# Optimization experiments

Measured on AMD Instinct MI355X. Metric: run time of the kernel, lower is better.

Reference implementation:

```python
import jax, jax.numpy as jnp
import numpy as np

N_HEAD = 12
N_EMBD = 768
HEAD_DIM = N_EMBD // N_HEAD


def setup_inputs() -> dict:
    key = jax.random.key(0)
    k1, k2, k3, k4, k5 = jax.random.split(key, 5)
    B, T, C = 1, 4096, N_EMBD
    s = 0.02
    return {
        "x": jax.random.normal(k1, (B, T, C), dtype=jnp.float32),
        "W_qkv": jax.random.normal(k2, (C, 3 * C), dtype=jnp.float32) * s,
        "b_qkv": jnp.zeros((3 * C,), dtype=jnp.float32),
        "W_out": jax.random.normal(k3, (C, C), dtype=jnp.float32) * s,
        "b_out": jnp.zeros((C,), dtype=jnp.float32),
    }


def reference(x, W_qkv, b_qkv, W_out, b_out):
    B, T, C = x.shape
    H, D = N_HEAD, HEAD_DIM
    qkv = x @ W_qkv + b_qkv                       # (B, T, 3C)
    qkv = qkv.reshape(B, T, 3, H, D)
    q = jnp.transpose(qkv[:, :, 0], (0, 2, 1, 3))  # (B, H, T, D)
    k = jnp.transpose(qkv[:, :, 1], (0, 2, 1, 3))
    v = jnp.transpose(qkv[:, :, 2], (0, 2, 1, 3))
    scores = jnp.einsum("bhqd,bhkd->bhqk", q, k) / jnp.sqrt(jnp.float32(D))
    causal = jnp.tril(jnp.ones((T, T), dtype=bool))
    scores = jnp.where(causal[None, None], scores, -jnp.inf)
    weights = jax.nn.softmax(scores, axis=-1)     # (B, H, T, T)
    out = jnp.einsum("bhqk,bhkd->bhqd", weights, v)
    out = jnp.transpose(out, (0, 2, 1, 3)).reshape(B, T, C)
    return out @ W_out + b_out
```

## Files before the change

kernel.cpp:

```cpp
#include <hip/hip_runtime.h>
#include <hip/hip_bf16.h>
#include <stdint.h>

#define T_SEQ 4096
#define C_EMB 768
#define C3    2304
#define CQK   1536
#define NH    12
#define HD    64
#define CH    16
#define NSLOT 1728

typedef __attribute__((ext_vector_type(8))) short short8;
typedef __attribute__((ext_vector_type(4))) short short4v;
typedef __attribute__((ext_vector_type(4))) float f32x4;

__device__ __forceinline__ short f2bf(float f) {
  __bf16 h = (__bf16)f;
  return __builtin_bit_cast(short, h);
}

__device__ __forceinline__ void gload_lds16(const void* g, void* l) {
  __builtin_amdgcn_global_load_lds((const __attribute__((address_space(1))) void*)g,
                                   (__attribute__((address_space(3))) void*)l, 16, 0, 0);
}

__global__ __launch_bounds__(256)
void cvt_kernel(const float* __restrict__ in, short* __restrict__ out, int n4) {
  int i = blockIdx.x * 256 + threadIdx.x;
  if (i < n4) {
    float4 v = ((const float4*)in)[i];
    short4v s = { f2bf(v.x), f2bf(v.y), f2bf(v.z), f2bf(v.w) };
    ((short4v*)out)[i] = s;
  }
}

__global__ __launch_bounds__(256)
void transpose_cvt_kernel(const float* __restrict__ W, short* __restrict__ WT,
                          int K, int N) {
  __shared__ float ts[32][33];
  const int r0 = blockIdx.y * 32, c0 = blockIdx.x * 32;
  const int tid = threadIdx.x;
  {
    int rr = tid >> 3, c4 = (tid & 7) * 4;
    float4 v = *(const float4*)(W + (size_t)(r0 + rr) * N + c0 + c4);
    ts[rr][c4 + 0] = v.x; ts[rr][c4 + 1] = v.y;
    ts[rr][c4 + 2] = v.z; ts[rr][c4 + 3] = v.w;
  }
  __syncthreads();
  {
    int nr = tid >> 3, k4 = (tid & 7) * 4;
    short4v s = { f2bf(ts[k4 + 0][nr]), f2bf(ts[k4 + 1][nr]),
                  f2bf(ts[k4 + 2][nr]), f2bf(ts[k4 + 3][nr]) };
    *(short4v*)(WT + (size_t)(c0 + nr) * K + r0 + k4) = s;
  }
}

template<int BN, bool SPLIT_V, bool OUT_F32>
__global__ __launch_bounds__(256)
void gemm_kernel(const short* __restrict__ A, const short* __restrict__ Bt,
                 const float* __restrict__ bias, void* __restrict__ Cp,
                 short* __restrict__ Vt, int N, int K) {
  constexpr int MF = (BN == 128) ? 4 : 2;
  __shared__ short As[128 * 32];
  __shared__ short Bs[BN * 32];
  const int row0 = blockIdx.y * 128, col0 = blockIdx.x * BN;
  const int tid = threadIdx.x, lane = tid & 63, wave = tid >> 6;
  const int lg = lane >> 4, lr = lane & 15;
  const int wr = (BN == 128) ? ((wave >> 1) * 64) : (wave * 32);
  const int wc = (BN == 128) ? ((wave & 1) * 64) : 0;

  f32x4 acc[MF][4];
  #pragma unroll
  for (int m_ = 0; m_ < MF; ++m_)
    #pragma unroll
    for (int n_ = 0; n_ < 4; ++n_) acc[m_][n_] = (f32x4){0.f, 0.f, 0.f, 0.f};

  const int srow = wave * 16 + (lane >> 2);
  const int scol = (lane & 3) * 8;

  for (int kt = 0; kt < K; kt += 32) {
    __syncthreads();
    #pragma unroll
    for (int c = 0; c < 2; ++c)
      gload_lds16(A + (size_t)(row0 + c * 64 + srow) * K + kt + scol,
                  As + c * 2048 + wave * 512);
    #pragma unroll
    for (int c = 0; c < BN / 64; ++c)
      gload_lds16(Bt + (size_t)(col0 + c * 64 + srow) * K + kt + scol,
                  Bs + c * 2048 + wave * 512);
    __syncthreads();

    short8 a[MF], b[4];
    #pragma unroll
    for (int m_ = 0; m_ < MF; ++m_)
      a[m_] = *(const short8*)&As[(wr + m_ * 16 + lr) * 32 + lg * 8];
    #pragma unroll
    for (int n_ = 0; n_ < 4; ++n_)
      b[n_] = *(const short8*)&Bs[(wc + n_ * 16 + lr) * 32 + lg * 8];
    #pragma unroll
    for (int m_ = 0; m_ < MF; ++m_)
      #pragma unroll
      for (int n_ = 0; n_ < 4; ++n_)
        acc[m_][n_] = __builtin_amdgcn_mfma_f32_16x16x32_bf16(a[m_], b[n_], acc[m_][n_], 0, 0, 0);
  }

  const bool isV = SPLIT_V && (col0 >= CQK);
  #pragma unroll
  for (int n_ = 0; n_ < 4; ++n_) {
    const int col = col0 + wc + n_ * 16 + lr;
    const float bv = bias[col];
    #pragma unroll
    for (int m_ = 0; m_ < MF; ++m_) {
      const int rbase = row0 + wr + m_ * 16 + lg * 4;
      if constexpr (OUT_F32) {
        #pragma unroll
        for (int r = 0; r < 4; ++r)
          ((float*)Cp)[(size_t)(rbase + r) * N + col] = acc[m_][n_][r] + bv;
      } else {
        if (!isV) {
          const int nout = SPLIT_V ? CQK : N;
          #pragma unroll
          for (int r = 0; r < 4; ++r)
            ((short*)Cp)[(size_t)(rbase + r) * nout + col] = f2bf(acc[m_][n_][r] + bv);
        } else {
          short4v p = { f2bf(acc[m_][n_][0] + bv), f2bf(acc[m_][n_][1] + bv),
                        f2bf(acc[m_][n_][2] + bv), f2bf(acc[m_][n_][3] + bv) };
          const int t64 = rbase & 63;
          const int p64 = (t64 & 32) + ((t64 & 12) << 1) + ((t64 & 16) >> 2);
          *(short4v*)(Vt + (size_t)(col - CQK) * T_SEQ + (rbase & ~63) + p64) = p;
        }
      }
    }
  }
}

__global__ __launch_bounds__(256, 2)
void attn_kernel(const short* __restrict__ qk, const short* __restrict__ Vt,
                 short* __restrict__ out, float* __restrict__ pO,
                 float* __restrict__ pML) {
  const int w = blockIdx.x * 4 + (threadIdx.x >> 6);
  const int lane = threadIdx.x & 63;
  const int h = w % NH;
  const int ii = 159 - w / NH;
  int qt, ck;
  if (ii < 16)      { qt = ii;                 ck = 0; }
  else if (ii < 48) { qt = 16 + (ii - 16) / 2; ck = (ii - 16) % 2; }
  else if (ii < 96) { qt = 32 + (ii - 48) / 3; ck = (ii - 48) % 3; }
  else              { qt = 48 + (ii - 96) / 4; ck = (ii - 96) % 4; }
  const int q0 = qt * 64;
  const int ntiles = qt + 1;
  const int t0 = ck * CH;
  const int rem = ntiles - t0;
  const int nloc = rem < CH ? rem : CH;

  const int lg = lane >> 4, lr = lane & 15;
  const float SC = 0.18033688011f;

  short8 qf[4][2];
  #pragma unroll
  for (int g = 0; g < 4; ++g)
    #pragma unroll
    for (int ks = 0; ks < 2; ++ks)
      qf[g][ks] = *(const short8*)(qk + (size_t)(q0 + g * 16 + lr) * CQK +
                                   h * HD + ks * 32 + lg * 8);

  float mrun[4], lrun[4];
  f32x4 o[4][4];
  #pragma unroll
  for (int g = 0; g < 4; ++g) { mrun[g] = -1e30f; lrun[g] = 0.f; }
  #pragma unroll
  for (int d = 0; d < 4; ++d)
    #pragma unroll
    for (int g = 0; g < 4; ++g) o[d][g] = (f32x4){0.f, 0.f, 0.f, 0.f};

  const short* kp[4];
  const short* vp[4];
  #pragma unroll
  for (int n = 0; n < 4; ++n)
    kp[n] = qk + C_EMB + h * HD + (size_t)(t0 * 64 + n * 16 + lr) * CQK + lg * 8;
  #pragma unroll
  for (int d = 0; d < 4; ++d)
    vp[d] = Vt + (size_t)(h * HD + d * 16 + lr) * T_SEQ + t0 * 64 + lg * 8;

  for (int tt = 0; tt < nloc; ++tt) {
    const int tl = t0 + tt;

    short8 kf[4][2], vf[4][2];
    #pragma unroll
    for (int n = 0; n < 4; ++n) {
      kf[n][0] = *(const short8*)(kp[n]);
      kf[n][1] = *(const short8*)(kp[n] + 32);
      vf[n][0] = *(const short8*)(vp[n]);
      vf[n][1] = *(const short8*)(vp[n] + 32);
      kp[n] += 64 * CQK;
      vp[n] += 64;
    }

    #pragma unroll
    for (int g = 0; g < 4; ++g) {
      f32x4 s[4];
      __builtin_amdgcn_s_setprio(1);
      #pragma unroll
      for (int n = 0; n < 4; ++n) {
        f32x4 cc = (f32x4){0.f, 0.f, 0.f, 0.f};
        #pragma unroll
        for (int ks = 0; ks < 2; ++ks)
          cc = __builtin_amdgcn_mfma_f32_16x16x32_bf16(kf[n][ks], qf[g][ks], cc, 0, 0, 0);
        s[n] = cc;
      }
      __builtin_amdgcn_s_setprio(0);

      if (tl == ntiles - 1) {
        #pragma unroll
        for (int n = 0; n < 4; ++n)
          #pragma unroll
          for (int r = 0; r < 4; ++r)
            if (n * 16 + lg * 4 + r > g * 16 + lr) s[n][r] = -1e30f;
      }

      float pmax = s[0][0];
      #pragma unroll
      for (int n = 0; n < 4; ++n)
        #pragma unroll
        for (int r = 0; r < 4; ++r) pmax = fmaxf(pmax, s[n][r]);
      pmax = fmaxf(pmax, __shfl_xor(pmax, 16));
      pmax = fmaxf(pmax, __shfl_xor(pmax, 32));

      if (!__all(pmax <= mrun[g] + 44.0f)) {
        const float mn = fmaxf(mrun[g], pmax);
        const float al = exp2f((mrun[g] - mn) * SC);
        lrun[g] *= al;
        #pragma unroll
        for (int d = 0; d < 4; ++d) o[d][g] *= al;
        mrun[g] = mn;
      }
      const float msc = mrun[g] * SC;

      float psum = 0.f;
      #pragma unroll
      for (int n = 0; n < 4; ++n)
        #pragma unroll
        for (int r = 0; r < 4; ++r) {
          float p = exp2f(fmaf(s[n][r], SC, -msc));
          s[n][r] = p;
          psum += p;
        }
      psum += __shfl_xor(psum, 16);
      psum += __shfl_xor(psum, 32);
      lrun[g] += psum;

      __builtin_amdgcn_s_setprio(1);
      #pragma unroll
      for (int ks = 0; ks < 2; ++ks) {
        short8 pb = { f2bf(s[2 * ks][0]),     f2bf(s[2 * ks][1]),
                      f2bf(s[2 * ks][2]),     f2bf(s[2 * ks][3]),
                      f2bf(s[2 * ks + 1][0]), f2bf(s[2 * ks + 1][1]),
                      f2bf(s[2 * ks + 1][2]), f2bf(s[2 * ks + 1][3]) };
        #pragma unroll
        for (int d = 0; d < 4; ++d)
          o[d][g] = __builtin_amdgcn_mfma_f32_16x16x32_bf16(vf[d][ks], pb, o[d][g], 0, 0, 0);
      }
      __builtin_amdgcn_s_setprio(0);
    }
  }

  if (qt < CH) {
    #pragma unroll
    for (int g = 0; g < 4; ++g) {
      const float linv = 1.f / lrun[g];
      const size_t qrow = q0 + g * 16 + lr;
      #pragma unroll
      for (int d = 0; d < 4; ++d) {
        short4v ov;
        #pragma unroll
        for (int r = 0; r < 4; ++r) ov[r] = f2bf(o[d][g][r] * linv);
        *(short4v*)(out + qrow * C_EMB + h * HD + d * 16 + lg * 4) = ov;
      }
    }
  } else {
    const int sbase = (qt < 32) ? 2 * (qt - 16)
                    : (qt < 48) ? 32 + 3 * (qt - 32)
                                : 80 + 4 * (qt - 48);
    const int slot = h * 144 + sbase + ck;
    #pragma unroll
    for (int g = 0; g < 4; ++g) {
      const int row = g * 16 + lr;
      float* po = pO + (size_t)slot * 4096 + row * 64;
      #pragma unroll
      for (int d = 0; d < 4; ++d)
        *(f32x4*)&po[d * 16 + lg * 4] = o[d][g];
      if (lg == 0) {
        pML[(size_t)slot * 128 + row * 2 + 0] = mrun[g];
        pML[(size_t)slot * 128 + row * 2 + 1] = lrun[g];
      }
    }
  }
}

__global__ __launch_bounds__(256)
void merge_kernel(const float* __restrict__ pO, const float* __restrict__ pML,
                  short* __restrict__ out) {
  const int bd = blockIdx.x;
  const int h = bd % NH;
  const int qt = 16 + bd / NH;
  const int nc = qt / CH + 1;
  const int sbase = (qt < 32) ? 2 * (qt - 16)
                  : (qt < 48) ? 32 + 3 * (qt - 32)
                              : 80 + 4 * (qt - 48);
  const int slot0 = h * 144 + sbase;
  const int tid = threadIdx.x;
  const int q = tid >> 2, dc = (tid & 3) << 4;
  const float SC = 0.18033688011f;

  float mi[4], li[4];
  float M = -1e30f;
  #pragma unroll
  for (int i = 0; i < 4; ++i)
    if (i < nc) {
      mi[i] = pML[(size_t)(slot0 + i) * 128 + q * 2 + 0];
      li[i] = pML[(size_t)(slot0 + i) * 128 + q * 2 + 1];
      M = fmaxf(M, mi[i]);
    }

  f32x4 O[4];
  #pragma unroll
  for (int d4 = 0; d4 < 4; ++d4) O[d4] = (f32x4){0.f, 0.f, 0.f, 0.f};
  float L = 0.f;
  #pragma unroll
  for (int i = 0; i < 4; ++i)
    if (i < nc) {
      const float a = exp2f((mi[i] - M) * SC);
      L = fmaf(li[i], a, L);
      const float* po = pO + (size_t)(slot0 + i) * 4096 + q * 64 + dc;
      #pragma unroll
      for (int d4 = 0; d4 < 4; ++d4) {
        f32x4 v = *(const f32x4*)(po + d4 * 4);
        #pragma unroll
        for (int r = 0; r < 4; ++r) O[d4][r] = fmaf(v[r], a, O[d4][r]);
      }
    }

  const float linv = 1.f / L;
  #pragma unroll
  for (int d4 = 0; d4 < 4; ++d4) {
    short4v ov;
    #pragma unroll
    for (int r = 0; r < 4; ++r) ov[r] = f2bf(O[d4][r] * linv);
    *(short4v*)(out + (size_t)(qt * 64 + q) * C_EMB + h * HD + dc + d4 * 4) = ov;
  }
}

extern "C" void kernel_launch(void* const* d_in, const int* in_sizes, int n_in,
                              void* d_out, int out_size, void* d_ws, size_t ws_size,
                              hipStream_t stream) {
  const float* x    = (const float*)d_in[0];
  const float* Wqkv = (const float*)d_in[1];
  const float* bqkv = (const float*)d_in[2];
  const float* Wout = (const float*)d_in[3];
  const float* bout = (const float*)d_in[4];

  short* xb    = (short*)d_ws;
  short* WqkvT = xb    + (size_t)T_SEQ * C_EMB;
  short* WoutT = WqkvT + (size_t)C3 * C_EMB;
  short* qk    = WoutT + (size_t)C_EMB * C_EMB;
  short* Vt    = qk    + (size_t)T_SEQ * CQK;
  float* pO    = (float*)(Vt + (size_t)C_EMB * T_SEQ);
  float* pML   = pO + (size_t)NSLOT * 4096;

  cvt_kernel<<<(T_SEQ * C_EMB / 4) / 256, 256, 0, stream>>>(x, xb, T_SEQ * C_EMB / 4);
  transpose_cvt_kernel<<<dim3(C3 / 32, C_EMB / 32), 256, 0, stream>>>(Wqkv, WqkvT, C_EMB, C3);
  transpose_cvt_kernel<<<dim3(C_EMB / 32, C_EMB / 32), 256, 0, stream>>>(Wout, WoutT, C_EMB, C_EMB);

  gemm_kernel<128, true, false><<<dim3(C3 / 128, T_SEQ / 128), 256, 0, stream>>>(
      xb, WqkvT, bqkv, qk, Vt, C3, C_EMB);

  attn_kernel<<<dim3(480), 256, 0, stream>>>(qk, Vt, xb, pO, pML);
  merge_kernel<<<dim3(NH * 48), 256, 0, stream>>>(pO, pML, xb);

  gemm_kernel<64, false, true><<<dim3(C_EMB / 64, T_SEQ / 128), 256, 0, stream>>>(
      xb, WoutT, bout, d_out, nullptr, C_EMB, C_EMB);
}
```

Measured before the change: 140.8 us.

## Store Q/K/V in MFMA-fragment layout and split query tile across two waves

The QKV GEMM epilogue now writes Q, K and V into a per-head, per-tile fragment-packed layout, so each lane's short8 operand sits contiguously and the attention kernel does fully coalesced 512-element-strided loads. The attention kernel also halves each wave's query rows (two waves per 64-row tile, 960 blocks), cutting accumulator registers and raising launch bounds to 3 blocks per SM. The trade-off is that K/V tiles are loaded twice, once per half-wave pair, and the GEMM epilogue does scattered 2-byte stores for Q/K.

New measurement: 130.2 us. 7.6% less time.

```diff
diff --git a/kernel.cpp b/kernel.cpp
--- a/kernel.cpp
+++ b/kernel.cpp
@@ -60,7 +60,8 @@
 __global__ __launch_bounds__(256)
 void gemm_kernel(const short* __restrict__ A, const short* __restrict__ Bt,
                  const float* __restrict__ bias, void* __restrict__ Cp,
-                 short* __restrict__ Vt, int N, int K) {
+                 short* __restrict__ Kfp, short* __restrict__ Vfp,
+                 int N, int K) {
   constexpr int MF = (BN == 128) ? 4 : 2;
   __shared__ short As[128 * 32];
   __shared__ short Bs[BN * 32];
@@ -105,6 +106,7 @@
         acc[m_][n_] = __builtin_amdgcn_mfma_f32_16x16x32_bf16(a[m_], b[n_], acc[m_][n_], 0, 0, 0);
   }
 
+  const bool isK = SPLIT_V && (col0 >= C_EMB) && (col0 < CQK);
   const bool isV = SPLIT_V && (col0 >= CQK);
   #pragma unroll
   for (int n_ = 0; n_ < 4; ++n_) {
@@ -117,32 +119,50 @@
         #pragma unroll
         for (int r = 0; r < 4; ++r)
           ((float*)Cp)[(size_t)(rbase + r) * N + col] = acc[m_][n_][r] + bv;
+      } else if constexpr (!SPLIT_V) {
+        #pragma unroll
+        for (int r = 0; r < 4; ++r)
+          ((short*)Cp)[(size_t)(rbase + r) * N + col] = f2bf(acc[m_][n_][r] + bv);
       } else {
         if (!isV) {
-          const int nout = SPLIT_V ? CQK : N;
+          const int fcol = col & 63;
+          const int hh = (col >> 6) - (isK ? (C_EMB >> 6) : 0);
+          const int ks = (fcol >> 5) & 1, lgf = (fcol >> 3) & 3, e = fcol & 7;
+          const int tile = rbase >> 6, pair = (rbase >> 4) & 3, lrt = rbase & 15;
+          short* base = isK ? Kfp : (short*)Cp;
+          const size_t idx =
+              ((((size_t)(hh * 64 + tile) * 8 + pair * 2 + ks) * 64) +
+               lgf * 16 + lrt) * 8 + e;
           #pragma unroll
           for (int r = 0; r < 4; ++r)
-            ((short*)Cp)[(size_t)(rbase + r) * nout + col] = f2bf(acc[m_][n_][r] + bv);
+            base[idx + r * 8] = f2bf(acc[m_][n_][r] + bv);
         } else {
-          short4v p = { f2bf(acc[m_][n_][0] + bv), f2bf(acc[m_][n_][1] + bv),
-                        f2bf(acc[m_][n_][2] + bv), f2bf(acc[m_][n_][3] + bv) };
+          const int dv = col - CQK;
+          const int hh = dv >> 6, fv = dv & 63, dd = fv >> 4, lrv = fv & 15;
           const int t64 = rbase & 63;
           const int p64 = (t64 & 32) + ((t64 & 12) << 1) + ((t64 & 16) >> 2);
-          *(short4v*)(Vt + (size_t)(col - CQK) * T_SEQ + (rbase & ~63) + p64) = p;
+          const int kt2 = rbase >> 6;
+          short4v pck = { f2bf(acc[m_][n_][0] + bv), f2bf(acc[m_][n_][1] + bv),
+                          f2bf(acc[m_][n_][2] + bv), f2bf(acc[m_][n_][3] + bv) };
+          const size_t idx =
+              ((((size_t)(hh * 64 + kt2) * 8 + dd * 2 + (p64 >> 5)) * 64) +
+               ((p64 >> 3) & 3) * 16 + lrv) * 8 + (p64 & 7);
+          *(short4v*)(Vfp + idx) = pck;
         }
       }
     }
   }
 }
 
-__global__ __launch_bounds__(256, 2)
-void attn_kernel(const short* __restrict__ qk, const short* __restrict__ Vt,
-                 short* __restrict__ out, float* __restrict__ pO,
-                 float* __restrict__ pML) {
-  const int w = blockIdx.x * 4 + (threadIdx.x >> 6);
+__global__ __launch_bounds__(256, 3)
+void attn_kernel(const short* __restrict__ Qf, const short* __restrict__ Kf,
+                 const short* __restrict__ Vf, short* __restrict__ out,
+                 float* __restrict__ pO, float* __restrict__ pML) {
+  const int jj = blockIdx.x * 4 + (threadIdx.x >> 6);
   const int lane = threadIdx.x & 63;
-  const int h = w % NH;
-  const int ii = 159 - w / NH;
+  const int pr = jj >> 1, qh = jj & 1;
+  const int h = pr % NH;
+  const int ii = 159 - pr / NH;
   int qt, ck;
   if (ii < 16)      { qt = ii;                 ck = 0; }
   else if (ii < 48) { qt = 16 + (ii - 16) / 2; ck = (ii - 16) % 2; }
@@ -157,48 +177,43 @@
   const int lg = lane >> 4, lr = lane & 15;
   const float SC = 0.18033688011f;
 
-  short8 qf[4][2];
-  #pragma unroll
-  for (int g = 0; g < 4; ++g)
+  const short* Qb = Qf + ((size_t)(h * 64 + qt) * 8) * 512 + lane * 8;
+  short8 qfr[2][2];
+  #pragma unroll
+  for (int g = 0; g < 2; ++g)
     #pragma unroll
     for (int ks = 0; ks < 2; ++ks)
-      qf[g][ks] = *(const short8*)(qk + (size_t)(q0 + g * 16 + lr) * CQK +
-                                   h * HD + ks * 32 + lg * 8);
-
-  float mrun[4], lrun[4];
-  f32x4 o[4][4];
-  #pragma unroll
-  for (int g = 0; g < 4; ++g) { mrun[g] = -1e30f; lrun[g] = 0.f; }
+      qfr[g][ks] = *(const short8*)(Qb + ((qh * 2 + g) * 2 + ks) * 512);
+
+  float mrun[2] = { -1e30f, -1e30f }, lrun[2] = { 0.f, 0.f };
+  f32x4 o[4][2];
   #pragma unroll
   for (int d = 0; d < 4; ++d)
     #pragma unroll
-    for (int g = 0; g < 4; ++g) o[d][g] = (f32x4){0.f, 0.f, 0.f, 0.f};
-
-  const short* kp[4];
-  const short* vp[4];
-  #pragma unroll
-  for (int n = 0; n < 4; ++n)
-    kp[n] = qk + C_EMB + h * HD + (size_t)(t0 * 64 + n * 16 + lr) * CQK + lg * 8;
-  #pragma unroll
-  for (int d = 0; d < 4; ++d)
-    vp[d] = Vt + (size_t)(h * HD + d * 16 + lr) * T_SEQ + t0 * 64 + lg * 8;
+    for (int g = 0; g < 2; ++g) o[d][g] = (f32x4){0.f, 0.f, 0.f, 0.f};
+
+  const short* Kp = Kf + ((size_t)(h * 64 + t0) * 8) * 512 + lane * 8;
+  const short* Vp = Vf + ((size_t)(h * 64 + t0) * 8) * 512 + lane * 8;
 
   for (int tt = 0; tt < nloc; ++tt) {
     const int tl = t0 + tt;
 
-    short8 kf[4][2], vf[4][2];
-    #pragma unroll
-    for (int n = 0; n < 4; ++n) {
-      kf[n][0] = *(const short8*)(kp[n]);
-      kf[n][1] = *(const short8*)(kp[n] + 32);
-      vf[n][0] = *(const short8*)(vp[n]);
-      vf[n][1] = *(const short8*)(vp[n] + 32);
-      kp[n] += 64 * CQK;
-      vp[n] += 64;
-    }
-
-    #pragma unroll
-    for (int g = 0; g < 4; ++g) {
+    short8 kf_[4][2], vf_[4][2];
+    #pragma unroll
+    for (int n = 0; n < 4; ++n)
+      #pragma unroll
+      for (int ks = 0; ks < 2; ++ks)
+        kf_[n][ks] = *(const short8*)(Kp + (n * 2 + ks) * 512);
+    #pragma unroll
+    for (int d = 0; d < 4; ++d)
+      #pragma unroll
+      for (int ks = 0; ks < 2; ++ks)
+        vf_[d][ks] = *(const short8*)(Vp + (d * 2 + ks) * 512);
+    Kp += 4096;
+    Vp += 4096;
+
+    #pragma unroll
+    for (int g = 0; g < 2; ++g) {
       f32x4 s[4];
       __builtin_amdgcn_s_setprio(1);
       #pragma unroll
@@ -206,7 +221,7 @@
         f32x4 cc = (f32x4){0.f, 0.f, 0.f, 0.f};
         #pragma unroll
         for (int ks = 0; ks < 2; ++ks)
-          cc = __builtin_amdgcn_mfma_f32_16x16x32_bf16(kf[n][ks], qf[g][ks], cc, 0, 0, 0);
+          cc = __builtin_amdgcn_mfma_f32_16x16x32_bf16(kf_[n][ks], qfr[g][ks], cc, 0, 0, 0);
         s[n] = cc;
       }
       __builtin_amdgcn_s_setprio(0);
@@ -216,7 +231,7 @@
         for (int n = 0; n < 4; ++n)
           #pragma unroll
           for (int r = 0; r < 4; ++r)
-            if (n * 16 + lg * 4 + r > g * 16 + lr) s[n][r] = -1e30f;
+            if (n * 16 + lg * 4 + r > qh * 32 + g * 16 + lr) s[n][r] = -1e30f;
       }
 
       float pmax = s[0][0];
@@ -259,7 +274,7 @@
                       f2bf(s[2 * ks + 1][2]), f2bf(s[2 * ks + 1][3]) };
         #pragma unroll
         for (int d = 0; d < 4; ++d)
-          o[d][g] = __builtin_amdgcn_mfma_f32_16x16x32_bf16(vf[d][ks], pb, o[d][g], 0, 0, 0);
+          o[d][g] = __builtin_amdgcn_mfma_f32_16x16x32_bf16(vf_[d][ks], pb, o[d][g], 0, 0, 0);
       }
       __builtin_amdgcn_s_setprio(0);
     }
@@ -267,9 +282,9 @@
 
   if (qt < CH) {
     #pragma unroll
-    for (int g = 0; g < 4; ++g) {
+    for (int g = 0; g < 2; ++g) {
       const float linv = 1.f / lrun[g];
-      const size_t qrow = q0 + g * 16 + lr;
+      const size_t qrow = q0 + qh * 32 + g * 16 + lr;
       #pragma unroll
       for (int d = 0; d < 4; ++d) {
         short4v ov;
@@ -284,8 +299,8 @@
                                 : 80 + 4 * (qt - 48);
     const int slot = h * 144 + sbase + ck;
     #pragma unroll
-    for (int g = 0; g < 4; ++g) {
-      const int row = g * 16 + lr;
+    for (int g = 0; g < 2; ++g) {
+      const int row = qh * 32 + g * 16 + lr;
       float* po = pO + (size_t)slot * 4096 + row * 64;
       #pragma unroll
       for (int d = 0; d < 4; ++d)
@@ -363,9 +378,10 @@
   short* xb    = (short*)d_ws;
   short* WqkvT = xb    + (size_t)T_SEQ * C_EMB;
   short* WoutT = WqkvT + (size_t)C3 * C_EMB;
-  short* qk    = WoutT + (size_t)C_EMB * C_EMB;
-  short* Vt    = qk    + (size_t)T_SEQ * CQK;
-  float* pO    = (float*)(Vt + (size_t)C_EMB * T_SEQ);
+  short* Qf    = WoutT + (size_t)C_EMB * C_EMB;
+  short* Kf    = Qf    + (size_t)T_SEQ * C_EMB;
+  short* Vf    = Kf    + (size_t)T_SEQ * C_EMB;
+  float* pO    = (float*)(Vf + (size_t)T_SEQ * C_EMB);
   float* pML   = pO + (size_t)NSLOT * 4096;
 
   cvt_kernel<<<(T_SEQ * C_EMB / 4) / 256, 256, 0, stream>>>(x, xb, T_SEQ * C_EMB / 4);
@@ -373,11 +389,11 @@
   transpose_cvt_kernel<<<dim3(C_EMB / 32, C_EMB / 32), 256, 0, stream>>>(Wout, WoutT, C_EMB, C_EMB);
 
   gemm_kernel<128, true, false><<<dim3(C3 / 128, T_SEQ / 128), 256, 0, stream>>>(
-      xb, WqkvT, bqkv, qk, Vt, C3, C_EMB);
-
-  attn_kernel<<<dim3(480), 256, 0, stream>>>(qk, Vt, xb, pO, pML);
+      xb, WqkvT, bqkv, Qf, Kf, Vf, C3, C_EMB);
+
+  attn_kernel<<<dim3(960), 256, 0, stream>>>(Qf, Kf, Vf, xb, pO, pML);
   merge_kernel<<<dim3(NH * 48), 256, 0, stream>>>(pO, pML, xb);
 
   gemm_kernel<64, false, true><<<dim3(C_EMB / 64, T_SEQ / 128), 256, 0, stream>>>(
-      xb, WoutT, bout, d_out, nullptr, C_EMB, C_EMB);
-}
+      xb, WoutT, bout, d_out, nullptr, nullptr, C_EMB, C_EMB);
+}
```
